# Kernel tuning notes

Measured on AMD Instinct MI355X. Metric: run time of the kernel, lower is better.

The kernel has to match this reference:

```python
import jax, jax.numpy as jnp
import numpy as np

N_NODES = 100000
N_EDGES = 1600000
IN_CH = 64
HID = 64
N_CLASSES = 10
N_GRAPHS = 64


def setup_inputs() -> dict:
    key = jax.random.key(0)
    ks = jax.random.split(key, 12)
    x = jax.random.normal(ks[0], (N_NODES, IN_CH), dtype=jnp.float32)
    edge_index = jax.random.randint(ks[1], (2, N_EDGES), 0, N_NODES, dtype=jnp.int64)
    batch = jnp.sort(jax.random.randint(ks[2], (N_NODES,), 0, N_GRAPHS, dtype=jnp.int64))

    def glorot(k, fan_in, fan_out):
        lim = jnp.sqrt(6.0 / (fan_in + fan_out))
        return jax.random.uniform(k, (fan_in, fan_out), jnp.float32, -lim, lim)

    W1 = glorot(ks[3], IN_CH, HID); b1 = jnp.zeros((HID,), jnp.float32)
    W2 = glorot(ks[4], HID, HID);   b2 = jnp.zeros((HID,), jnp.float32)
    W3 = glorot(ks[5], HID, HID);   b3 = jnp.zeros((HID,), jnp.float32)
    Wc = glorot(ks[6], HID, N_CLASSES)
    bc = jnp.zeros((N_CLASSES,), jnp.float32)
    return {"x": x, "edge_index": edge_index, "batch": batch,
            "W1": W1, "b1": b1, "W2": W2, "b2": b2, "W3": W3, "b3": b3,
            "Wc": Wc, "bc": bc}


def _gcn_conv(x, W, b, src, dst, edge_norm, self_norm):
    # x' = D^-1/2 (A+I) D^-1/2 (x W) + b  (PyG GCNConv with self-loops)
    h = x @ W                                    # [N, H] small GEMM
    msg = h[src] * edge_norm[:, None]            # [E, H] gather (memory-bound)
    agg = jax.ops.segment_sum(msg, dst, num_segments=N_NODES)  # scatter-add
    agg = agg + h * self_norm[:, None]           # self-loop contribution
    return agg + b


def reference(x, edge_index, batch, W1, b1, W2, b2, W3, b3, Wc, bc):
    src, dst = edge_index[0], edge_index[1]
    # degree on target nodes including self-loop (PyG gcn_norm)
    deg = jax.ops.segment_sum(jnp.ones((N_EDGES,), x.dtype), dst,
                              num_segments=N_NODES) + 1.0
    dinv = jnp.where(deg > 0, deg ** -0.5, 0.0)
    edge_norm = dinv[src] * dinv[dst]            # [E]
    self_norm = dinv * dinv                      # [N]

    h = jax.nn.relu(_gcn_conv(x, W1, b1, src, dst, edge_norm, self_norm))
    h = jax.nn.relu(_gcn_conv(h, W2, b2, src, dst, edge_norm, self_norm))
    h = jax.nn.relu(_gcn_conv(h, W3, b3, src, dst, edge_norm, self_norm))

    # global mean pool per graph
    sums = jax.ops.segment_sum(h, batch, num_segments=N_GRAPHS)       # [G, H]
    cnts = jax.ops.segment_sum(jnp.ones((N_NODES,), h.dtype), batch,
                               num_segments=N_GRAPHS)
    graph_emb = sums / jnp.maximum(cnts, 1.0)[:, None]
    return graph_emb @ Wc + bc                   # [G, num_classes]
```

## Files before the change

kernel.cpp:

```cpp
#include <hip/hip_runtime.h>


#define HIDDEN 64
#define BSHIFT 8
#define MAXB 512
#define BCAP 5120

typedef __attribute__((ext_vector_type(8))) short bf16x8;
typedef __attribute__((ext_vector_type(4))) float f32x4;

__device__ __forceinline__ unsigned short f32_to_bf16_rne(float f) {
    unsigned u = __float_as_uint(f);
    u += 0x7FFF + ((u >> 16) & 1);
    return (unsigned short)(u >> 16);
}
__device__ __forceinline__ float bf16_to_f32(unsigned short h) {
    return __uint_as_float((unsigned)h << 16);
}

__global__ __launch_bounds__(256) void scatter_onepass(const int* __restrict__ src,
                                                       const int* __restrict__ dst,
                                                       int* __restrict__ gCursor,
                                                       unsigned* __restrict__ rec,
                                                       int E, int perBlock) {
    __shared__ int hist[MAXB];
    __shared__ int cur[MAXB];
    for (int i = threadIdx.x; i < MAXB; i += 256) hist[i] = 0;
    __syncthreads();
    int beg = blockIdx.x * perBlock;
    int end = min(beg + perBlock, E);
    if (beg >= end) return;
    int n4 = (end - beg) >> 2;
    const int4* d4 = reinterpret_cast<const int4*>(dst + beg);
    const int4* s4 = reinterpret_cast<const int4*>(src + beg);
    for (int g = threadIdx.x; g < n4; g += 256) {
        int4 d = d4[g];
        atomicAdd(&hist[d.x >> BSHIFT], 1);
        atomicAdd(&hist[d.y >> BSHIFT], 1);
        atomicAdd(&hist[d.z >> BSHIFT], 1);
        atomicAdd(&hist[d.w >> BSHIFT], 1);
    }
    for (int e = beg + (n4 << 2) + threadIdx.x; e < end; e += 256)
        atomicAdd(&hist[dst[e] >> BSHIFT], 1);
    __syncthreads();
    for (int i = threadIdx.x; i < MAXB; i += 256)
        cur[i] = hist[i] ? (i * BCAP + atomicAdd(&gCursor[i], hist[i])) : 0;
    __syncthreads();
    for (int g = threadIdx.x; g < n4; g += 256) {
        int4 d = d4[g];
        int4 s = s4[g];
        int p;
        p = atomicAdd(&cur[d.x >> BSHIFT], 1); rec[p] = ((unsigned)s.x << 8) | (unsigned)(d.x & 255);
        p = atomicAdd(&cur[d.y >> BSHIFT], 1); rec[p] = ((unsigned)s.y << 8) | (unsigned)(d.y & 255);
        p = atomicAdd(&cur[d.z >> BSHIFT], 1); rec[p] = ((unsigned)s.z << 8) | (unsigned)(d.z & 255);
        p = atomicAdd(&cur[d.w >> BSHIFT], 1); rec[p] = ((unsigned)s.w << 8) | (unsigned)(d.w & 255);
    }
    for (int e = beg + (n4 << 2) + threadIdx.x; e < end; e += 256) {
        int d = dst[e];
        int p = atomicAdd(&cur[d >> BSHIFT], 1);
        rec[p] = ((unsigned)src[e] << 8) | (unsigned)(d & 255);
    }
}

__global__ __launch_bounds__(256) void bucket_build(const unsigned* __restrict__ rec,
                                                    const int* __restrict__ gCursor,
                                                    int* __restrict__ rowBeg,
                                                    int* __restrict__ rowEnd,
                                                    float* __restrict__ dinv,
                                                    int* __restrict__ col, int N) {
    int b = blockIdx.x;
    int base = b * BCAP, cnt = gCursor[b];
    int t = threadIdx.x;
    __shared__ int hist[256];
    __shared__ int sc[256];
    __shared__ int cur[256];
    hist[t] = 0;
    __syncthreads();
    for (int i = base + t; i < base + cnt; i += 256)
        atomicAdd(&hist[rec[i] & 255], 1);
    __syncthreads();
    int myCnt = hist[t];
    sc[t] = myCnt;
    __syncthreads();
    for (int off = 1; off < 256; off <<= 1) {
        int u = (t >= off) ? sc[t - off] : 0;
        __syncthreads();
        sc[t] += u;
        __syncthreads();
    }
    int nodeBase = base + sc[t] - myCnt;
    int node = (b << BSHIFT) + t;
    if (node < N) {
        rowBeg[node] = nodeBase;
        rowEnd[node] = nodeBase + myCnt;
        dinv[node] = rsqrtf((float)(myCnt + 1));
    }
    cur[t] = nodeBase;
    __syncthreads();
    for (int i = base + t; i < base + cnt; i += 256) {
        unsigned r = rec[i];
        int p = atomicAdd(&cur[r & 255], 1);
        col[p] = (int)(r >> 8);
    }
}

template<bool F32IN>
__global__ __launch_bounds__(256) void gemm_mfma(const void* __restrict__ Xin,
                                                 const float* __restrict__ W,
                                                 const float* __restrict__ dinv,
                                                 unsigned short* __restrict__ Hs, int N) {
    __shared__ __align__(16) unsigned short A_t[64][72];
    __shared__ __align__(16) unsigned short Wh_t[64][72];
    __shared__ __align__(16) unsigned short Wl_t[64][72];
    int t = threadIdx.x;
    int rowBase = blockIdx.x * 64;
    for (int i = t; i < 4096; i += 256) {
        int k = i >> 6, c = i & 63;
        float w = W[i];
        unsigned short h = f32_to_bf16_rne(w);
        float rem = w - bf16_to_f32(h);
        Wh_t[c][k] = h;
        Wl_t[c][k] = f32_to_bf16_rne(rem);
    }
    for (int c = t; c < 512; c += 256) {
        int r = c >> 3, kc = c & 7;
        int rr = min(rowBase + r, N - 1);
        if (F32IN) {
            const float4* xp = reinterpret_cast<const float4*>((const float*)Xin + ((size_t)rr << 6)) + kc * 2;
            float4 a = xp[0], b = xp[1];
            unsigned v0 = f32_to_bf16_rne(a.x) | ((unsigned)f32_to_bf16_rne(a.y) << 16);
            unsigned v1 = f32_to_bf16_rne(a.z) | ((unsigned)f32_to_bf16_rne(a.w) << 16);
            unsigned v2 = f32_to_bf16_rne(b.x) | ((unsigned)f32_to_bf16_rne(b.y) << 16);
            unsigned v3 = f32_to_bf16_rne(b.z) | ((unsigned)f32_to_bf16_rne(b.w) << 16);
            *reinterpret_cast<uint4*>(&A_t[r][kc * 8]) = make_uint4(v0, v1, v2, v3);
        } else {
            uint4 v = reinterpret_cast<const uint4*>((const unsigned short*)Xin + ((size_t)rr << 6))[kc];
            *reinterpret_cast<uint4*>(&A_t[r][kc * 8]) = v;
        }
    }
    __syncthreads();
    int w = t >> 6, lane = t & 63;
    int lr = lane & 15, lk = lane >> 4;
    int arow = w * 16 + lr;
    f32x4 zero = {0.f, 0.f, 0.f, 0.f};
    f32x4 acc[4];
    acc[0] = zero; acc[1] = zero; acc[2] = zero; acc[3] = zero;
    bf16x8 a0 = *reinterpret_cast<const bf16x8*>(&A_t[arow][lk * 8]);
    bf16x8 a1 = *reinterpret_cast<const bf16x8*>(&A_t[arow][32 + lk * 8]);
#pragma unroll
    for (int ct = 0; ct < 4; ct++) {
        int bcol = ct * 16 + lr;
        bf16x8 bh0 = *reinterpret_cast<const bf16x8*>(&Wh_t[bcol][lk * 8]);
        bf16x8 bl0 = *reinterpret_cast<const bf16x8*>(&Wl_t[bcol][lk * 8]);
        bf16x8 bh1 = *reinterpret_cast<const bf16x8*>(&Wh_t[bcol][32 + lk * 8]);
        bf16x8 bl1 = *reinterpret_cast<const bf16x8*>(&Wl_t[bcol][32 + lk * 8]);
        acc[ct] = __builtin_amdgcn_mfma_f32_16x16x32_bf16(a0, bh0, acc[ct], 0, 0, 0);
        acc[ct] = __builtin_amdgcn_mfma_f32_16x16x32_bf16(a0, bl0, acc[ct], 0, 0, 0);
        acc[ct] = __builtin_amdgcn_mfma_f32_16x16x32_bf16(a1, bh1, acc[ct], 0, 0, 0);
        acc[ct] = __builtin_amdgcn_mfma_f32_16x16x32_bf16(a1, bl1, acc[ct], 0, 0, 0);
    }
#pragma unroll
    for (int i = 0; i < 4; i++) {
        int row = rowBase + w * 16 + lk * 4 + i;
        if (row < N) {
            float dn = dinv[row];
#pragma unroll
            for (int ct = 0; ct < 4; ct++) {
                Hs[(size_t)row * 64 + ct * 16 + lr] = f32_to_bf16_rne(dn * acc[ct][i]);
            }
        }
    }
}

__global__ __launch_bounds__(256) void aggregate_kernel(const unsigned short* __restrict__ Hs,
                                                        const int* __restrict__ rowBeg,
                                                        const int* __restrict__ rowEnd,
                                                        const int* __restrict__ col,
                                                        const float* __restrict__ dinv,
                                                        const float* __restrict__ bias,
                                                        unsigned short* __restrict__ OUT, int N) {
    int node = blockIdx.x * 4 + (threadIdx.x >> 6);
    int lane = threadIdx.x & 63;
    if (node >= N) return;
    int beg = __builtin_amdgcn_readfirstlane(rowBeg[node]);
    int end = __builtin_amdgcn_readfirstlane(rowEnd[node]);
    float a0 = 0.f, a1 = 0.f, a2 = 0.f, a3 = 0.f;
    float a4 = 0.f, a5 = 0.f, a6 = 0.f, a7 = 0.f;
    int e = beg;
    for (; e + 8 <= end; e += 8) {
        int s0 = col[e],     s1 = col[e + 1], s2 = col[e + 2], s3 = col[e + 3];
        int s4 = col[e + 4], s5 = col[e + 5], s6 = col[e + 6], s7 = col[e + 7];
        unsigned short v0 = Hs[(size_t)s0 * 64 + lane];
        unsigned short v1 = Hs[(size_t)s1 * 64 + lane];
        unsigned short v2 = Hs[(size_t)s2 * 64 + lane];
        unsigned short v3 = Hs[(size_t)s3 * 64 + lane];
        unsigned short v4 = Hs[(size_t)s4 * 64 + lane];
        unsigned short v5 = Hs[(size_t)s5 * 64 + lane];
        unsigned short v6 = Hs[(size_t)s6 * 64 + lane];
        unsigned short v7 = Hs[(size_t)s7 * 64 + lane];
        a0 += bf16_to_f32(v0); a1 += bf16_to_f32(v1);
        a2 += bf16_to_f32(v2); a3 += bf16_to_f32(v3);
        a4 += bf16_to_f32(v4); a5 += bf16_to_f32(v5);
        a6 += bf16_to_f32(v6); a7 += bf16_to_f32(v7);
    }
    for (; e < end; e++) a0 += bf16_to_f32(Hs[(size_t)col[e] * 64 + lane]);
    float acc = ((a0 + a1) + (a2 + a3)) + ((a4 + a5) + (a6 + a7));
    acc += bf16_to_f32(Hs[(size_t)node * 64 + lane]);
    acc = fmaxf(acc * dinv[node] + bias[lane], 0.f);
    OUT[(size_t)node * 64 + lane] = f32_to_bf16_rne(acc);
}

__global__ __launch_bounds__(256) void pool_partial(const unsigned short* __restrict__ H,
                                                    const int* __restrict__ batch,
                                                    float* __restrict__ sums, int N) {
    int wid = (blockIdx.x * blockDim.x + threadIdx.x) >> 6;
    int lane = threadIdx.x & 63;
    int start = wid * 64;
    if (start >= N) return;
    int end = min(start + 64, N);
    int g = batch[start];
    float acc = 0.f;
    for (int n = start; n < end; n++) {
        int bg = batch[n];
        if (bg != g) { atomicAdd(&sums[g * 64 + lane], acc); acc = 0.f; g = bg; }
        acc += bf16_to_f32(H[(size_t)n * 64 + lane]);
    }
    atomicAdd(&sums[g * 64 + lane], acc);
}

__device__ __forceinline__ int lower_bound_dev(const int* a, int n, int key) {
    int lo = 0, hi = n;
    while (lo < hi) { int mid = (lo + hi) >> 1; if (a[mid] < key) lo = mid + 1; else hi = mid; }
    return lo;
}

__global__ void classify_kernel(const float* __restrict__ sums, const float* __restrict__ Wc,
                                const float* __restrict__ bc, const int* __restrict__ batch,
                                float* __restrict__ out, int N) {
    int t = blockIdx.x * blockDim.x + threadIdx.x;
    if (t >= 64 * 10) return;
    int g = t / 10, c = t % 10;
    float acc = 0.f;
    for (int k = 0; k < 64; k++) acc += sums[g * 64 + k] * Wc[k * 10 + c];
    int cnt = lower_bound_dev(batch, N, g + 1) - lower_bound_dev(batch, N, g);
    out[t] = acc / (float)max(cnt, 1) + bc[c];
}

extern "C" void kernel_launch(void* const* d_in, const int* in_sizes, int n_in,
                              void* d_out, int out_size, void* d_ws, size_t ws_size,
                              hipStream_t stream) {
    const float* x  = (const float*)d_in[0];
    const int* ei   = (const int*)d_in[1];
    const int* batch= (const int*)d_in[2];
    const float* W1 = (const float*)d_in[3];
    const float* b1 = (const float*)d_in[4];
    const float* W2 = (const float*)d_in[5];
    const float* b2 = (const float*)d_in[6];
    const float* W3 = (const float*)d_in[7];
    const float* b3 = (const float*)d_in[8];
    const float* Wc = (const float*)d_in[9];
    const float* bc = (const float*)d_in[10];

    int N = in_sizes[0] / HIDDEN;
    int E = in_sizes[1] / 2;
    const int* src = ei;
    const int* dst = ei + E;
    int NB = (N + 255) >> 8;

    char* ws = (char*)d_ws;
    size_t off = 0;
    auto alloc = [&](size_t bytes) { void* p = ws + off; off = (off + bytes + 255) & ~(size_t)255; return p; };
    int*   gCursor= (int*)  alloc((size_t)MAXB * 4);
    int*   rowBeg = (int*)  alloc((size_t)N * 4);
    int*   rowEnd = (int*)  alloc((size_t)N * 4);
    float* dinv   = (float*)alloc((size_t)N * 4);
    int*   col    = (int*)  alloc((size_t)NB * BCAP * 4);
    unsigned short* hb = (unsigned short*)alloc((size_t)N * HIDDEN * 2);
    unsigned short* ha = (unsigned short*)alloc((size_t)N * HIDDEN * 2);
    float* sums   = (float*)alloc(64 * 64 * 4);
    unsigned* rec = (unsigned*)alloc((size_t)NB * BCAP * 4);

    int grid = 256;
    int perBlock = (((E + grid - 1) / grid) + 3) & ~3;
    hipMemsetAsync(gCursor, 0, (size_t)MAXB * 4, stream);
    hipMemsetAsync(sums, 0, 64 * 64 * 4, stream);
    scatter_onepass<<<grid, 256, 0, stream>>>(src, dst, gCursor, rec, E, perBlock);
    bucket_build<<<NB, 256, 0, stream>>>(rec, gCursor, rowBeg, rowEnd, dinv, col, N);

    int gGemm = (N + 63) / 64;
    int gAgg  = (N + 3) / 4;
    gemm_mfma<true><<<gGemm, 256, 0, stream>>>(x, W1, dinv, hb, N);
    aggregate_kernel<<<gAgg, 256, 0, stream>>>(hb, rowBeg, rowEnd, col, dinv, b1, ha, N);
    gemm_mfma<false><<<gGemm, 256, 0, stream>>>(ha, W2, dinv, hb, N);
    aggregate_kernel<<<gAgg, 256, 0, stream>>>(hb, rowBeg, rowEnd, col, dinv, b2, ha, N);
    gemm_mfma<false><<<gGemm, 256, 0, stream>>>(ha, W3, dinv, hb, N);
    aggregate_kernel<<<gAgg, 256, 0, stream>>>(hb, rowBeg, rowEnd, col, dinv, b3, ha, N);

    pool_partial<<<(N + 255) / 256, 256, 0, stream>>>(ha, batch, sums, N);
    classify_kernel<<<1, 640, 0, stream>>>(sums, Wc, bc, batch, (float*)d_out, N);
}
```

Before: 273.5 us.

## Load GEMM A operands directly to registers, process two tiles per block, prefetch indices

The GEMM kernel no longer stages the input tile in shared memory. Each lane loads its A fragments straight from global memory into registers, and each block now covers 128 rows in two tiles, so the split W staging is amortised over twice as many rows. The aggregate kernel software-pipelines its column-index loads, fetching the next 8 indices while the current 8 gathers are issued, to hide index-load latency. The risks are halving the GEMM grid, which reduces parallelism, and extra register pressure in the aggregation loop.

```diff
diff --git a/kernel.cpp b/kernel.cpp
--- a/kernel.cpp
+++ b/kernel.cpp
@@ -109,64 +109,68 @@
                                                  const float* __restrict__ W,
                                                  const float* __restrict__ dinv,
                                                  unsigned short* __restrict__ Hs, int N) {
-    __shared__ __align__(16) unsigned short A_t[64][72];
     __shared__ __align__(16) unsigned short Wh_t[64][72];
     __shared__ __align__(16) unsigned short Wl_t[64][72];
     int t = threadIdx.x;
-    int rowBase = blockIdx.x * 64;
     for (int i = t; i < 4096; i += 256) {
         int k = i >> 6, c = i & 63;
         float w = W[i];
         unsigned short h = f32_to_bf16_rne(w);
-        float rem = w - bf16_to_f32(h);
         Wh_t[c][k] = h;
-        Wl_t[c][k] = f32_to_bf16_rne(rem);
-    }
-    for (int c = t; c < 512; c += 256) {
-        int r = c >> 3, kc = c & 7;
-        int rr = min(rowBase + r, N - 1);
-        if (F32IN) {
-            const float4* xp = reinterpret_cast<const float4*>((const float*)Xin + ((size_t)rr << 6)) + kc * 2;
-            float4 a = xp[0], b = xp[1];
-            unsigned v0 = f32_to_bf16_rne(a.x) | ((unsigned)f32_to_bf16_rne(a.y) << 16);
-            unsigned v1 = f32_to_bf16_rne(a.z) | ((unsigned)f32_to_bf16_rne(a.w) << 16);
-            unsigned v2 = f32_to_bf16_rne(b.x) | ((unsigned)f32_to_bf16_rne(b.y) << 16);
-            unsigned v3 = f32_to_bf16_rne(b.z) | ((unsigned)f32_to_bf16_rne(b.w) << 16);
-            *reinterpret_cast<uint4*>(&A_t[r][kc * 8]) = make_uint4(v0, v1, v2, v3);
-        } else {
-            uint4 v = reinterpret_cast<const uint4*>((const unsigned short*)Xin + ((size_t)rr << 6))[kc];
-            *reinterpret_cast<uint4*>(&A_t[r][kc * 8]) = v;
-        }
+        Wl_t[c][k] = f32_to_bf16_rne(w - bf16_to_f32(h));
     }
     __syncthreads();
     int w = t >> 6, lane = t & 63;
     int lr = lane & 15, lk = lane >> 4;
-    int arow = w * 16 + lr;
-    f32x4 zero = {0.f, 0.f, 0.f, 0.f};
-    f32x4 acc[4];
-    acc[0] = zero; acc[1] = zero; acc[2] = zero; acc[3] = zero;
-    bf16x8 a0 = *reinterpret_cast<const bf16x8*>(&A_t[arow][lk * 8]);
-    bf16x8 a1 = *reinterpret_cast<const bf16x8*>(&A_t[arow][32 + lk * 8]);
+    int rowBase = blockIdx.x * 128;
 #pragma unroll
-    for (int ct = 0; ct < 4; ct++) {
-        int bcol = ct * 16 + lr;
-        bf16x8 bh0 = *reinterpret_cast<const bf16x8*>(&Wh_t[bcol][lk * 8]);
-        bf16x8 bl0 = *reinterpret_cast<const bf16x8*>(&Wl_t[bcol][lk * 8]);
-        bf16x8 bh1 = *reinterpret_cast<const bf16x8*>(&Wh_t[bcol][32 + lk * 8]);
-        bf16x8 bl1 = *reinterpret_cast<const bf16x8*>(&Wl_t[bcol][32 + lk * 8]);
-        acc[ct] = __builtin_amdgcn_mfma_f32_16x16x32_bf16(a0, bh0, acc[ct], 0, 0, 0);
-        acc[ct] = __builtin_amdgcn_mfma_f32_16x16x32_bf16(a0, bl0, acc[ct], 0, 0, 0);
-        acc[ct] = __builtin_amdgcn_mfma_f32_16x16x32_bf16(a1, bh1, acc[ct], 0, 0, 0);
-        acc[ct] = __builtin_amdgcn_mfma_f32_16x16x32_bf16(a1, bl1, acc[ct], 0, 0, 0);
-    }
+    for (int tile = 0; tile < 2; tile++) {
+        int arow = rowBase + tile * 64 + w * 16 + lr;
+        int rr = min(arow, N - 1);
+        bf16x8 a0, a1;
+        if (F32IN) {
+            const float* xp = (const float*)Xin + ((size_t)rr << 6) + lk * 8;
+            float4 p0 = *reinterpret_cast<const float4*>(xp);
+            float4 p1 = *reinterpret_cast<const float4*>(xp + 4);
+            float4 p2 = *reinterpret_cast<const float4*>(xp + 32);
+            float4 p3 = *reinterpret_cast<const float4*>(xp + 36);
+            a0[0] = (short)f32_to_bf16_rne(p0.x); a0[1] = (short)f32_to_bf16_rne(p0.y);
+            a0[2] = (short)f32_to_bf16_rne(p0.z); a0[3] = (short)f32_to_bf16_rne(p0.w);
+            a0[4] = (short)f32_to_bf16_rne(p1.x); a0[5] = (short)f32_to_bf16_rne(p1.y);
+            a0[6] = (short)f32_to_bf16_rne(p1.z); a0[7] = (short)f32_to_bf16_rne(p1.w);
+            a1[0] = (short)f32_to_bf16_rne(p2.x); a1[1] = (short)f32_to_bf16_rne(p2.y);
+            a1[2] = (short)f32_to_bf16_rne(p2.z); a1[3] = (short)f32_to_bf16_rne(p2.w);
+            a1[4] = (short)f32_to_bf16_rne(p3.x); a1[5] = (short)f32_to_bf16_rne(p3.y);
+            a1[6] = (short)f32_to_bf16_rne(p3.z); a1[7] = (short)f32_to_bf16_rne(p3.w);
+        } else {
+            const unsigned short* xp = (const unsigned short*)Xin + ((size_t)rr << 6) + lk * 8;
+            a0 = *reinterpret_cast<const bf16x8*>(xp);
+            a1 = *reinterpret_cast<const bf16x8*>(xp + 32);
+        }
+        f32x4 zero = {0.f, 0.f, 0.f, 0.f};
+        f32x4 acc[4];
+        acc[0] = zero; acc[1] = zero; acc[2] = zero; acc[3] = zero;
 #pragma unroll
-    for (int i = 0; i < 4; i++) {
-        int row = rowBase + w * 16 + lk * 4 + i;
-        if (row < N) {
-            float dn = dinv[row];
+        for (int ct = 0; ct < 4; ct++) {
+            int bcol = ct * 16 + lr;
+            bf16x8 bh0 = *reinterpret_cast<const bf16x8*>(&Wh_t[bcol][lk * 8]);
+            bf16x8 bl0 = *reinterpret_cast<const bf16x8*>(&Wl_t[bcol][lk * 8]);
+            bf16x8 bh1 = *reinterpret_cast<const bf16x8*>(&Wh_t[bcol][32 + lk * 8]);
+            bf16x8 bl1 = *reinterpret_cast<const bf16x8*>(&Wl_t[bcol][32 + lk * 8]);
+            acc[ct] = __builtin_amdgcn_mfma_f32_16x16x32_bf16(a0, bh0, acc[ct], 0, 0, 0);
+            acc[ct] = __builtin_amdgcn_mfma_f32_16x16x32_bf16(a0, bl0, acc[ct], 0, 0, 0);
+            acc[ct] = __builtin_amdgcn_mfma_f32_16x16x32_bf16(a1, bh1, acc[ct], 0, 0, 0);
+            acc[ct] = __builtin_amdgcn_mfma_f32_16x16x32_bf16(a1, bl1, acc[ct], 0, 0, 0);
+        }
 #pragma unroll
-            for (int ct = 0; ct < 4; ct++) {
-                Hs[(size_t)row * 64 + ct * 16 + lr] = f32_to_bf16_rne(dn * acc[ct][i]);
+        for (int i = 0; i < 4; i++) {
+            int row = rowBase + tile * 64 + w * 16 + lk * 4 + i;
+            if (row < N) {
+                float dn = dinv[row];
+#pragma unroll
+                for (int ct = 0; ct < 4; ct++) {
+                    Hs[(size_t)row * 64 + ct * 16 + lr] = f32_to_bf16_rne(dn * acc[ct][i]);
+                }
             }
         }
     }
@@ -187,21 +191,34 @@
     float a0 = 0.f, a1 = 0.f, a2 = 0.f, a3 = 0.f;
     float a4 = 0.f, a5 = 0.f, a6 = 0.f, a7 = 0.f;
     int e = beg;
-    for (; e + 8 <= end; e += 8) {
-        int s0 = col[e],     s1 = col[e + 1], s2 = col[e + 2], s3 = col[e + 3];
-        int s4 = col[e + 4], s5 = col[e + 5], s6 = col[e + 6], s7 = col[e + 7];
-        unsigned short v0 = Hs[(size_t)s0 * 64 + lane];
-        unsigned short v1 = Hs[(size_t)s1 * 64 + lane];
-        unsigned short v2 = Hs[(size_t)s2 * 64 + lane];
-        unsigned short v3 = Hs[(size_t)s3 * 64 + lane];
-        unsigned short v4 = Hs[(size_t)s4 * 64 + lane];
-        unsigned short v5 = Hs[(size_t)s5 * 64 + lane];
-        unsigned short v6 = Hs[(size_t)s6 * 64 + lane];
-        unsigned short v7 = Hs[(size_t)s7 * 64 + lane];
-        a0 += bf16_to_f32(v0); a1 += bf16_to_f32(v1);
-        a2 += bf16_to_f32(v2); a3 += bf16_to_f32(v3);
-        a4 += bf16_to_f32(v4); a5 += bf16_to_f32(v5);
-        a6 += bf16_to_f32(v6); a7 += bf16_to_f32(v7);
+    if (e + 8 <= end) {
+        int c0 = col[e],     c1 = col[e + 1], c2 = col[e + 2], c3 = col[e + 3];
+        int c4 = col[e + 4], c5 = col[e + 5], c6 = col[e + 6], c7 = col[e + 7];
+        while (true) {
+            int en = e + 8;
+            bool more = (en + 8 <= end);
+            int n0, n1, n2, n3, n4, n5, n6, n7;
+            if (more) {
+                n0 = col[en];     n1 = col[en + 1]; n2 = col[en + 2]; n3 = col[en + 3];
+                n4 = col[en + 4]; n5 = col[en + 5]; n6 = col[en + 6]; n7 = col[en + 7];
+            }
+            unsigned short v0 = Hs[(size_t)c0 * 64 + lane];
+            unsigned short v1 = Hs[(size_t)c1 * 64 + lane];
+            unsigned short v2 = Hs[(size_t)c2 * 64 + lane];
+            unsigned short v3 = Hs[(size_t)c3 * 64 + lane];
+            unsigned short v4 = Hs[(size_t)c4 * 64 + lane];
+            unsigned short v5 = Hs[(size_t)c5 * 64 + lane];
+            unsigned short v6 = Hs[(size_t)c6 * 64 + lane];
+            unsigned short v7 = Hs[(size_t)c7 * 64 + lane];
+            a0 += bf16_to_f32(v0); a1 += bf16_to_f32(v1);
+            a2 += bf16_to_f32(v2); a3 += bf16_to_f32(v3);
+            a4 += bf16_to_f32(v4); a5 += bf16_to_f32(v5);
+            a6 += bf16_to_f32(v6); a7 += bf16_to_f32(v7);
+            e = en;
+            if (!more) break;
+            c0 = n0; c1 = n1; c2 = n2; c3 = n3;
+            c4 = n4; c5 = n5; c6 = n6; c7 = n7;
+        }
     }
     for (; e < end; e++) a0 += bf16_to_f32(Hs[(size_t)col[e] * 64 + lane]);
     float acc = ((a0 + a1) + (a2 + a3)) + ((a4 + a5) + (a6 + a7));
@@ -287,7 +304,7 @@
     scatter_onepass<<<grid, 256, 0, stream>>>(src, dst, gCursor, rec, E, perBlock);
     bucket_build<<<NB, 256, 0, stream>>>(rec, gCursor, rowBeg, rowEnd, dinv, col, N);
 
-    int gGemm = (N + 63) / 64;
+    int gGemm = (N + 127) / 128;
     int gAgg  = (N + 3) / 4;
     gemm_mfma<true><<<gGemm, 256, 0, stream>>>(x, W1, dinv, hb, N);
     aggregate_kernel<<<gAgg, 256, 0, stream>>>(hb, rowBeg, rowEnd, col, dinv, b1, ha, N);
```

Measured after the change: 269.3 us. Within noise of the previous version (-1.5%).
